# Kernel tuning notes

Hardware: AMD Instinct MI355X
Metric: run time of the kernel (lower is better)

The kernel has to match this reference:

```python
import jax, jax.numpy as jnp
import numpy as np
from jax import lax

D_MODEL = 1024
D_INNER = 2048   # expand * d_model
D_STATE = 16
D_CONV = 4
DT_RANK = 64     # ceil(d_model / 16)
B_SZ, L_SEQ = 2, 2048


def setup_inputs() -> dict:
    key = jax.random.key(0)
    ks = jax.random.split(key, 12)
    s = lambda *sh: 1.0 / np.sqrt(sh[-1])
    inp = {
        "x": jax.random.normal(ks[0], (B_SZ, L_SEQ, D_MODEL), jnp.float32),
        "in_proj_w": jax.random.normal(ks[1], (2 * D_INNER, D_MODEL), jnp.float32) * s(D_MODEL),
        "conv_w": jax.random.normal(ks[2], (D_INNER, 1, D_CONV), jnp.float32) * 0.3,
        "conv_b": jax.random.normal(ks[3], (D_INNER,), jnp.float32) * 0.05,
        "x_proj_w": jax.random.normal(ks[4], (DT_RANK + 2 * D_STATE, D_INNER), jnp.float32) * s(D_INNER),
        "dt_proj_w": jax.random.normal(ks[5], (D_INNER, DT_RANK), jnp.float32) * s(DT_RANK),
        "dt_proj_b": jnp.log(jnp.exp(jax.random.uniform(ks[6], (D_INNER,), jnp.float32, 1e-3, 1e-1)) - 1.0),
        "A_log": jnp.log(jnp.broadcast_to(jnp.arange(1, D_STATE + 1, dtype=jnp.float32), (D_INNER, D_STATE))),
        "D": jnp.ones((D_INNER,), jnp.float32),
        "out_proj_w": jax.random.normal(ks[7], (D_MODEL, D_INNER), jnp.float32) * s(D_INNER),
        "ln_w": jnp.ones((D_MODEL,), jnp.float32),
        "ln_b": jnp.zeros((D_MODEL,), jnp.float32),
    }
    return inp


def _mamba(x, in_proj_w, conv_w, conv_b, x_proj_w, dt_proj_w, dt_proj_b, A_log, D, out_proj_w):
    # x: [B, L, d_model]
    xz = x @ in_proj_w.T                             # [B, L, 2*d_inner]
    u, z = jnp.split(xz, 2, axis=-1)                 # [B, L, d_inner] each
    # depthwise causal conv1d along L
    u_c = jnp.swapaxes(u, 1, 2)                      # [B, d_inner, L]
    u_c = lax.conv_general_dilated(
        u_c, conv_w, window_strides=(1,), padding=[(D_CONV - 1, 0)],
        feature_group_count=D_INNER, dimension_numbers=("NCH", "OIH", "NCH"))
    u_c = u_c + conv_b[None, :, None]
    u_c = jax.nn.silu(jnp.swapaxes(u_c, 1, 2))       # [B, L, d_inner]
    # input-dependent dt, B, C
    x_dbl = u_c @ x_proj_w.T                         # [B, L, dt_rank + 2*d_state]
    dt_lr = x_dbl[..., :DT_RANK]
    Bm = x_dbl[..., DT_RANK:DT_RANK + D_STATE]       # [B, L, d_state]
    Cm = x_dbl[..., DT_RANK + D_STATE:]              # [B, L, d_state]
    dt = jax.nn.softplus(dt_lr @ dt_proj_w.T + dt_proj_b)  # [B, L, d_inner]
    A = -jnp.exp(A_log)                              # [d_inner, d_state]

    def step(h, inputs):
        dt_t, b_t, c_t, u_t = inputs                 # [B,d_inner],[B,N],[B,N],[B,d_inner]
        dA = jnp.exp(dt_t[:, :, None] * A)           # [B, d_inner, N]
        h = h * dA + (dt_t * u_t)[:, :, None] * b_t[:, None, :]
        y_t = jnp.einsum("bdn,bn->bd", h, c_t)
        return h, y_t

    h0 = jnp.zeros((x.shape[0], D_INNER, D_STATE), x.dtype)
    xs = (jnp.swapaxes(dt, 0, 1), jnp.swapaxes(Bm, 0, 1),
          jnp.swapaxes(Cm, 0, 1), jnp.swapaxes(u_c, 0, 1))
    _, ys = lax.scan(step, h0, xs)                   # ys: [L, B, d_inner]
    y = jnp.swapaxes(ys, 0, 1) + u_c * D             # skip connection D*u
    y = y * jax.nn.silu(z)                           # gate
    return y @ out_proj_w.T                          # [B, L, d_model]


def _layernorm(x, w, b, eps=1e-5):
    mu = jnp.mean(x, axis=-1, keepdims=True)
    var = jnp.mean(jnp.square(x - mu), axis=-1, keepdims=True)
    return (x - mu) * lax.rsqrt(var + eps) * w + b


def reference(x, in_proj_w, conv_w, conv_b, x_proj_w, dt_proj_w, dt_proj_b,
              A_log, D, out_proj_w, ln_w, ln_b):
    y = _mamba(x, in_proj_w, conv_w, conv_b, x_proj_w, dt_proj_w, dt_proj_b,
               A_log, D, out_proj_w)
    return _layernorm(y + x, ln_w, ln_b)  # dropout_level=0 -> identity
```

## Files before the change

kernel.cpp:

```cpp
#include <hip/hip_runtime.h>
#include <hip/hip_bf16.h>
#include <math.h>

#define DEV static __device__ __forceinline__

typedef __hip_bfloat16 bf16;
typedef __attribute__((ext_vector_type(8))) short bf16x8;
typedef __attribute__((ext_vector_type(4))) short bf16x4;
typedef __attribute__((ext_vector_type(4))) float f32x4;

static constexpr int D_MODEL = 1024;
static constexpr int D_INNER = 2048;
static constexpr int D_STATE = 16;
static constexpr int DT_RANK = 64;
static constexpr int B_SZ   = 2;
static constexpr int L_SEQ  = 2048;
static constexpr int T_TOK  = B_SZ * L_SEQ;
static constexpr int LC     = 64;
static constexpr int NC     = L_SEQ / LC;
static constexpr int NXP    = DT_RANK + 2 * D_STATE;
static constexpr int KSPLIT = 8;

static constexpr int P_CONVW = 0;
static constexpr int P_CONVB = 8192;
static constexpr int P_DTB   = 10240;
static constexpr int P_ALOG  = 12288;
static constexpr int P_DW    = 45056;
static constexpr int P_LNW   = 47104;
static constexpr int P_LNB   = 48128;
static constexpr int P_TOT   = 49152;

DEV float bf2f(bf16 x) { return __bfloat162float(x); }
DEV bf16  f2bf(float x) { return __float2bfloat16(x); }
DEV float sigmoidf_(float x) { return 1.0f / (1.0f + __expf(-x)); }
DEV float s2f(short s) { bf16 b; __builtin_memcpy(&b, &s, 2); return bf2f(b); }
DEV short f2s(float x) { bf16 b = f2bf(x); short s; __builtin_memcpy(&s, &b, 2); return s; }

DEV bool probe_f32(const unsigned short* probe) { return probe[1] == 0; }

DEV void async_copy16(const void* g, void* l) {
  __builtin_amdgcn_global_load_lds(
      (const __attribute__((address_space(1))) void*)g,
      (__attribute__((address_space(3))) void*)l, 16, 0, 0);
}

template <int N>
DEV void vm_wait() {
  if constexpr (N == 6) asm volatile("s_waitcnt vmcnt(6)" ::: "memory");
  else                  asm volatile("s_waitcnt vmcnt(0)" ::: "memory");
}

__global__ void cvt_all(const void* s0, const void* s1, const void* s2,
                        const void* s3, const void* s4,
                        const void* s5, const void* s6, const void* s7,
                        const void* s8, const void* s9, const void* s10,
                        const void* s11,
                        bf16* d0, bf16* d1, bf16* d2, bf16* d3, bf16* d4,
                        float* params,
                        const unsigned short* __restrict__ probe)
{
  long i = (long)(blockIdx.x * 256 + threadIdx.x) * 8;
  const void* src; long off;
  bf16* dstb = nullptr; float* dstf = nullptr;
  if      (i <  4194304) { src = s0;  dstb = d0; off = i; }
  else if (i <  8388608) { src = s1;  dstb = d1; off = i - 4194304; }
  else if (i <  8585216) { src = s2;  dstb = d2; off = i - 8388608; }
  else if (i <  8716288) { src = s3;  dstb = d3; off = i - 8585216; }
  else if (i < 10813440) { src = s4;  dstb = d4; off = i - 8716288; }
  else if (i < 10821632) { src = s5;  dstf = params + P_CONVW; off = i - 10813440; }
  else if (i < 10823680) { src = s6;  dstf = params + P_CONVB; off = i - 10821632; }
  else if (i < 10825728) { src = s7;  dstf = params + P_DTB;   off = i - 10823680; }
  else if (i < 10858496) { src = s8;  dstf = params + P_ALOG;  off = i - 10825728; }
  else if (i < 10860544) { src = s9;  dstf = params + P_DW;    off = i - 10858496; }
  else if (i < 10861568) { src = s10; dstf = params + P_LNW;   off = i - 10860544; }
  else if (i < 10862592) { src = s11; dstf = params + P_LNB;   off = i - 10861568; }
  else return;
  bool isf32 = probe_f32(probe);
  float v[8];
  if (isf32) {
    float4 a = *(const float4*)((const float*)src + off);
    float4 b = *(const float4*)((const float*)src + off + 4);
    v[0]=a.x; v[1]=a.y; v[2]=a.z; v[3]=a.w;
    v[4]=b.x; v[5]=b.y; v[6]=b.z; v[7]=b.w;
  } else {
    bf16x8 t = *(const bf16x8*)((const bf16*)src + off);
    #pragma unroll
    for (int k = 0; k < 8; ++k) { short sk = t[k]; v[k] = s2f(sk); }
  }
  if (dstb) {
    bf16x8 o;
    #pragma unroll
    for (int k = 0; k < 8; ++k) o[k] = f2s(v[k]);
    *(bf16x8*)(dstb + off) = o;
  } else {
    f32x4 a = {v[0], v[1], v[2], v[3]};
    f32x4 b = {v[4], v[5], v[6], v[7]};
    *(f32x4*)(dstf + off)     = a;
    *(f32x4*)(dstf + off + 4) = b;
  }
}

static constexpr int SLOT = 48 * 1024;
static constexpr int BOFF = 32 * 1024;

DEV void stage_A(const bf16* __restrict__ A, int ld, int bm, int k0,
                 char* slot, int tid) {
  #pragma unroll
  for (int j = 0; j < 4; ++j) {
    int p   = j * 8192 + tid * 16;
    int row = p >> 7;
    int ck  = ((p >> 4) & 7) ^ (row & 7);
    async_copy16(A + (size_t)(bm + row) * ld + k0 + ck * 8,
                 slot + j * 8192 + (tid >> 6) * 1024);
  }
}

DEV void stage_B(const bf16* __restrict__ B, int ld, int bn, int k0,
                 char* slot, int tid) {
  #pragma unroll
  for (int j = 0; j < 2; ++j) {
    int p   = j * 8192 + tid * 16;
    int row = p >> 7;
    int ck  = ((p >> 4) & 7) ^ (row & 7);
    async_copy16(B + (size_t)(bn + row) * ld + k0 + ck * 8,
                 slot + BOFF + j * 8192 + (tid >> 6) * 1024);
  }
}

template <int MODE>
DEV void gemm_pipe(const bf16* __restrict__ A, const bf16* __restrict__ B,
                   int M, int K, int ld,
                   void* __restrict__ o0, void* __restrict__ o1,
                   const float* __restrict__ cw, const float* __restrict__ cb,
                   bf16* __restrict__ ufirst, bf16* __restrict__ ulast)
{
  __shared__ __align__(16) char ring[3 * SLOT];
  if (MODE == 3) {
    A += (size_t)blockIdx.z * K;
    B += (size_t)blockIdx.z * K;
  }
  const int tid  = threadIdx.x;
  const int wave = tid >> 6;
  const int lane = tid & 63;
  const int bm = blockIdx.x * 256;
  const int bn = blockIdx.y * 128;
  const int wm = (wave >> 1) * 64;
  const int wn = (wave & 1) * 64;
  const int fr = lane & 15;
  const int fq = lane >> 4;
  const int NT = K / 64;

  f32x4 acc[4][4];
  #pragma unroll
  for (int i = 0; i < 4; ++i)
    #pragma unroll
    for (int j = 0; j < 4; ++j)
      #pragma unroll
      for (int r = 0; r < 4; ++r) acc[i][j][r] = 0.0f;

  stage_A(A, ld, bm, 0,  ring,        tid);
  stage_B(B, ld, bn, 0,  ring,        tid);
  stage_A(A, ld, bm, 64, ring + SLOT, tid);
  stage_B(B, ld, bn, 64, ring + SLOT, tid);

  int scur = 0;
  #pragma unroll 1
  for (int tk = 0; tk < NT; ++tk) {
    if (tk < NT - 1) vm_wait<6>();
    else             vm_wait<0>();
    __builtin_amdgcn_sched_barrier(0);
    __builtin_amdgcn_s_barrier();
    __builtin_amdgcn_sched_barrier(0);

    const char* sa = ring + scur * SLOT;
    int snxt = scur + 2; if (snxt >= 3) snxt -= 3;
    char* sn = ring + snxt * SLOT;

    bf16x8 af[4][2], bg[2][2];
    #pragma unroll
    for (int mi = 0; mi < 4; ++mi)
      #pragma unroll
      for (int kk = 0; kk < 2; ++kk) {
        int row = wm + mi * 16 + fr;
        af[mi][kk] = *(const bf16x8*)(sa + row * 128 + (((kk * 4 + fq) ^ (fr & 7)) * 16));
      }
    #pragma unroll
    for (int ni = 0; ni < 2; ++ni)
      #pragma unroll
      for (int kk = 0; kk < 2; ++kk) {
        int row = wn + ni * 16 + fr;
        bg[ni][kk] = *(const bf16x8*)(sa + BOFF + row * 128 + (((kk * 4 + fq) ^ (fr & 7)) * 16));
      }
    __builtin_amdgcn_sched_barrier(0);
    if (tk + 2 < NT) stage_A(A, ld, bm, (tk + 2) * 64, sn, tid);
    __builtin_amdgcn_sched_barrier(0);
    asm volatile("s_waitcnt lgkmcnt(0)" ::: "memory");
    __builtin_amdgcn_sched_barrier(0);
    __builtin_amdgcn_s_setprio(1);
    #pragma unroll
    for (int kk = 0; kk < 2; ++kk)
      #pragma unroll
      for (int mi = 0; mi < 4; ++mi)
        #pragma unroll
        for (int ni = 0; ni < 2; ++ni)
          acc[mi][ni] = __builtin_amdgcn_mfma_f32_16x16x32_bf16(af[mi][kk], bg[ni][kk], acc[mi][ni], 0, 0, 0);
    __builtin_amdgcn_s_setprio(0);
    __builtin_amdgcn_sched_barrier(0);

    bf16x8 bh[2][2];
    #pragma unroll
    for (int ni = 0; ni < 2; ++ni)
      #pragma unroll
      for (int kk = 0; kk < 2; ++kk) {
        int row = wn + (ni + 2) * 16 + fr;
        bh[ni][kk] = *(const bf16x8*)(sa + BOFF + row * 128 + (((kk * 4 + fq) ^ (fr & 7)) * 16));
      }
    __builtin_amdgcn_sched_barrier(0);
    if (tk + 2 < NT) stage_B(B, ld, bn, (tk + 2) * 64, sn, tid);
    __builtin_amdgcn_sched_barrier(0);
    asm volatile("s_waitcnt lgkmcnt(0)" ::: "memory");
    __builtin_amdgcn_sched_barrier(0);
    __builtin_amdgcn_s_setprio(1);
    #pragma unroll
    for (int kk = 0; kk < 2; ++kk)
      #pragma unroll
      for (int mi = 0; mi < 4; ++mi)
        #pragma unroll
        for (int ni = 0; ni < 2; ++ni)
          acc[mi][ni + 2] = __builtin_amdgcn_mfma_f32_16x16x32_bf16(af[mi][kk], bh[ni][kk], acc[mi][ni + 2], 0, 0, 0);
    __builtin_amdgcn_s_setprio(0);
    __builtin_amdgcn_sched_barrier(0);

    scur = (scur + 1 == 3) ? 0 : scur + 1;
  }

  const int er = (lane >> 4) * 4;
  const int ec = lane & 15;

  if (MODE == 3) {
    #pragma unroll
    for (int mi = 0; mi < 4; ++mi)
      #pragma unroll
      for (int ni = 0; ni < 4; ++ni)
        #pragma unroll
        for (int r = 0; r < 4; ++r) {
          int row = bm + wm + mi * 16 + er + r;
          int col = bn + wn + ni * 16 + ec;
          ((bf16*)o0)[((size_t)blockIdx.z * M + row) * D_MODEL + col] = f2bf(acc[mi][ni][r]);
        }
    return;
  }

  if (bn >= D_INNER) {
    #pragma unroll
    for (int mi = 0; mi < 4; ++mi)
      #pragma unroll
      for (int ni = 0; ni < 4; ++ni)
        #pragma unroll
        for (int r = 0; r < 4; ++r) {
          int row = bm + wm + mi * 16 + er + r;
          int col = bn + wn + ni * 16 + ec - D_INNER;
          float v = acc[mi][ni][r];
          ((bf16*)o1)[(size_t)row * D_INNER + col] = f2bf(v * sigmoidf_(v));
        }
    return;
  }

  __syncthreads();
  bf16*  uT  = (bf16*)ring;
  float* cws = (float*)(ring + 70656);
  float* cbs = (float*)(ring + 72704);

  #pragma unroll
  for (int mi = 0; mi < 4; ++mi)
    #pragma unroll
    for (int ni = 0; ni < 4; ++ni)
      #pragma unroll
      for (int r = 0; r < 4; ++r)
        uT[(size_t)(wm + mi * 16 + er + r) * 136 + wn + ni * 16 + ec] = f2bf(acc[mi][ni][r]);

  if (tid < 128) {
    *(f32x4*)(cws + tid * 4) = *(const f32x4*)(cw + (size_t)(bn + tid) * 4);
    cbs[tid] = cb[bn + tid];
  }
  __syncthreads();

  if (tid < 48) {
    int i  = tid >> 4;
    int c8 = (tid & 15) * 8;
    size_t hb = ((size_t)(bm >> 8) * 3 + i) * D_INNER + bn + c8;
    *(bf16x8*)(ufirst + hb) = *(const bf16x8*)(uT + (size_t)i * 136 + c8);
    *(bf16x8*)(ulast  + hb) = *(const bf16x8*)(uT + (size_t)(253 + i) * 136 + c8);
  }

  const int cg = tid & 15;
  float cwr[4][8], cbr[8];
  #pragma unroll
  for (int i = 0; i < 8; ++i) {
    f32x4 w4 = *(const f32x4*)(cws + (cg * 8 + i) * 4);
    cwr[0][i] = w4[0]; cwr[1][i] = w4[1]; cwr[2][i] = w4[2]; cwr[3][i] = w4[3];
    cbr[i] = cbs[cg * 8 + i];
  }
  const int lbase = bm & (L_SEQ - 1);
  #pragma unroll
  for (int j = 0; j < 8; ++j) {
    int row = (tid >> 4) + j * 32;
    if (row < 3 && lbase != 0) continue;
    float a8[8];
    #pragma unroll
    for (int i = 0; i < 8; ++i) a8[i] = cbr[i];
    #pragma unroll
    for (int w = 0; w < 4; ++w) {
      if (row - 3 + w >= 0) {
        bf16x8 u8 = *(const bf16x8*)(uT + (size_t)(row - 3 + w) * 136 + cg * 8);
        #pragma unroll
        for (int i = 0; i < 8; ++i) { short uu = u8[i]; a8[i] += s2f(uu) * cwr[w][i]; }
      }
    }
    bf16x8 o;
    #pragma unroll
    for (int i = 0; i < 8; ++i) o[i] = f2s(a8[i] * sigmoidf_(a8[i]));
    *(bf16x8*)((bf16*)o0 + (size_t)(bm + row) * D_INNER + bn + cg * 8) = o;
  }
}

__global__ void __launch_bounds__(256) k_convfix(
    const bf16* __restrict__ ufirst, const bf16* __restrict__ ulast,
    const float* __restrict__ cw, const float* __restrict__ cb,
    bf16* __restrict__ uc_bf)
{
  int idx = blockIdx.x * 256 + threadIdx.x;
  int e4 = idx * 4;
  int ti = e4 >> 11;
  int c4 = e4 & 2047;
  int tb = ti / 3, r = ti - tb * 3;
  int rb = (tb < 7) ? tb + 1 : tb + 2;
  int token = rb * 256 + r;
  float a[4];
  float4 wv[4];
  #pragma unroll
  for (int i = 0; i < 4; ++i) {
    a[i]  = cb[c4 + i];
    wv[i] = *(const float4*)(cw + (size_t)(c4 + i) * 4);
  }
  #pragma unroll
  for (int w = 0; w < 4; ++w) {
    int g = r - 3 + w;
    const bf16* srcrow = (g < 0)
        ? (ulast  + ((size_t)(rb - 1) * 3 + (g + 3)) * D_INNER)
        : (ufirst + ((size_t)rb * 3 + g) * D_INNER);
    bf16x4 u = *(const bf16x4*)(srcrow + c4);
    #pragma unroll
    for (int i = 0; i < 4; ++i) { short su = u[i]; a[i] += s2f(su) * ((const float*)&wv[i])[w]; }
  }
  bf16x4 o;
  #pragma unroll
  for (int i = 0; i < 4; ++i) o[i] = f2s(a[i] * sigmoidf_(a[i]));
  *(bf16x4*)(uc_bf + (size_t)token * D_INNER + c4) = o;
}

__global__ void __launch_bounds__(256) k_xproj(const bf16* __restrict__ A,
                                               const bf16* __restrict__ B,
                                               float* __restrict__ o0)
{
  __shared__ __align__(16) bf16 As[128 * 32];
  __shared__ __align__(16) bf16 Bs[128 * 32];
  const int M = T_TOK, N = NXP, K = D_INNER / KSPLIT, ld = D_INNER;
  A += (size_t)blockIdx.z * K;
  B += (size_t)blockIdx.z * K;
  const int tid  = threadIdx.x;
  const int wave = tid >> 6;
  const int lane = tid & 63;
  const int bm = blockIdx.x * 128;
  const int bn = 0;
  const int wm = (wave >> 1) * 64;
  const int wn = (wave & 1) * 64;

  f32x4 acc[4][4];
  #pragma unroll
  for (int i = 0; i < 4; ++i)
    #pragma unroll
    for (int j = 0; j < 4; ++j)
      #pragma unroll
      for (int r = 0; r < 4; ++r) acc[i][j][r] = 0.0f;

  const int ar0 = tid >> 2;
  const int ar1 = ar0 + 64;
  const int ac  = (tid & 3) * 8;
  const int fr = lane & 15;
  const int fk = (lane >> 4) * 8;

  for (int k0 = 0; k0 < K; k0 += 32) {
    bf16x8 a0 = *(const bf16x8*)(A + (size_t)(bm + ar0) * ld + k0 + ac);
    bf16x8 a1 = *(const bf16x8*)(A + (size_t)(bm + ar1) * ld + k0 + ac);
    int r0 = bn + ar0; if (r0 > N - 1) r0 = N - 1;
    int r1 = bn + ar1; if (r1 > N - 1) r1 = N - 1;
    bf16x8 b0 = *(const bf16x8*)(B + (size_t)r0 * ld + k0 + ac);
    bf16x8 b1 = *(const bf16x8*)(B + (size_t)r1 * ld + k0 + ac);
    __syncthreads();
    *(bf16x8*)(As + ar0 * 32 + ac) = a0;
    *(bf16x8*)(As + ar1 * 32 + ac) = a1;
    *(bf16x8*)(Bs + ar0 * 32 + ac) = b0;
    *(bf16x8*)(Bs + ar1 * 32 + ac) = b1;
    __syncthreads();

    bf16x8 af[4], bg[4];
    #pragma unroll
    for (int mi = 0; mi < 4; ++mi)
      af[mi] = *(const bf16x8*)(As + (wm + mi * 16 + fr) * 32 + fk);
    #pragma unroll
    for (int ni = 0; ni < 4; ++ni)
      bg[ni] = *(const bf16x8*)(Bs + (wn + ni * 16 + fr) * 32 + fk);
    #pragma unroll
    for (int mi = 0; mi < 4; ++mi)
      #pragma unroll
      for (int ni = 0; ni < 4; ++ni)
        acc[mi][ni] = __builtin_amdgcn_mfma_f32_16x16x32_bf16(af[mi], bg[ni], acc[mi][ni], 0, 0, 0);
  }

  const int er = (lane >> 4) * 4;
  const int ec = lane & 15;
  #pragma unroll
  for (int mi = 0; mi < 4; ++mi)
    #pragma unroll
    for (int ni = 0; ni < 4; ++ni)
      #pragma unroll
      for (int r = 0; r < 4; ++r) {
        int row = bm + wm + mi * 16 + er + r;
        int col = bn + wn + ni * 16 + ec;
        if (col >= N) continue;
        o0[((size_t)blockIdx.z * M + row) * N + col] = acc[mi][ni][r];
      }
}

__global__ void __launch_bounds__(512) k_inproj(const bf16* A, const bf16* B,
    void* o0, void* o1, const float* cw, const float* cb,
    bf16* ufirst, bf16* ulast) {
  gemm_pipe<0>(A, B, T_TOK, D_MODEL, D_MODEL, o0, o1, cw, cb, ufirst, ulast);
}
__global__ void __launch_bounds__(512) k_outproj(const bf16* A, const bf16* B,
    void* o0) {
  gemm_pipe<3>(A, B, T_TOK, D_INNER / 2, D_INNER, o0, nullptr, nullptr, nullptr,
               nullptr, nullptr);
}

__global__ __launch_bounds__(256) void k_dtfuse(
    const float* __restrict__ partials,
    const bf16*  __restrict__ dtw,
    const float* __restrict__ dtbias,
    float* __restrict__ Bbuf, float* __restrict__ Cbuf,
    bf16* __restrict__ dtb)
{
  __shared__ __align__(16) bf16 Al[128 * 72];
  __shared__ __align__(16) bf16 Bl[128 * 72];
  const int tid = threadIdx.x;
  unsigned lin = blockIdx.x + gridDim.x * blockIdx.y;
  unsigned nid = (lin & 7) * 64 + (lin >> 3);
  const int cblk = nid & 15;
  const int tblk = nid >> 4;
  const int r0 = tblk * 128;
  const int c0 = cblk * 128;

  #pragma unroll
  for (int it = 0; it < 8; ++it) {
    int idx = it * 256 + tid;
    int row = idx >> 4;
    int g   = idx & 15;
    f32x4 s = {0.0f, 0.0f, 0.0f, 0.0f};
    #pragma unroll
    for (int kz = 0; kz < KSPLIT; ++kz)
      s += *(const f32x4*)(partials + ((size_t)kz * T_TOK + r0 + row) * NXP + g * 4);
    bf16x4 o;
    #pragma unroll
    for (int k = 0; k < 4; ++k) o[k] = f2s(s[k]);
    *(bf16x4*)(Al + row * 72 + g * 4) = o;
  }
  if (cblk == 0) {
    #pragma unroll
    for (int it = 0; it < 4; ++it) {
      int idx = it * 256 + tid;
      int row = idx >> 3;
      int g   = 16 + (idx & 7);
      f32x4 s = {0.0f, 0.0f, 0.0f, 0.0f};
      #pragma unroll
      for (int kz = 0; kz < KSPLIT; ++kz)
        s += *(const f32x4*)(partials + ((size_t)kz * T_TOK + r0 + row) * NXP + g * 4);
      if (g < 20) *(f32x4*)(Bbuf + (size_t)(r0 + row) * D_STATE + (g - 16) * 4) = s;
      else        *(f32x4*)(Cbuf + (size_t)(r0 + row) * D_STATE + (g - 20) * 4) = s;
    }
  }
  #pragma unroll
  for (int it = 0; it < 4; ++it) {
    int idx = it * 256 + tid;
    int row = idx >> 3;
    int cv  = (idx & 7) * 8;
    *(bf16x8*)(Bl + row * 72 + cv) = *(const bf16x8*)(dtw + (size_t)(c0 + row) * 64 + cv);
  }
  __syncthreads();

  const int wave = tid >> 6;
  const int lane = tid & 63;
  const int wm = (wave >> 1) * 64;
  const int wn = (wave & 1) * 64;
  const int fr = lane & 15;
  const int fk = (lane >> 4) * 8;
  const int er = (lane >> 4) * 4;
  const int ec = lane & 15;

  f32x4 acc[4][4];
  #pragma unroll
  for (int i = 0; i < 4; ++i)
    #pragma unroll
    for (int j = 0; j < 4; ++j)
      #pragma unroll
      for (int r = 0; r < 4; ++r) acc[i][j][r] = 0.0f;

  #pragma unroll
  for (int k0 = 0; k0 < 64; k0 += 32) {
    bf16x8 af[4], bg[4];
    #pragma unroll
    for (int mi = 0; mi < 4; ++mi)
      af[mi] = *(const bf16x8*)(Al + (wm + mi * 16 + fr) * 72 + k0 + fk);
    #pragma unroll
    for (int ni = 0; ni < 4; ++ni)
      bg[ni] = *(const bf16x8*)(Bl + (wn + ni * 16 + fr) * 72 + k0 + fk);
    #pragma unroll
    for (int mi = 0; mi < 4; ++mi)
      #pragma unroll
      for (int ni = 0; ni < 4; ++ni)
        acc[mi][ni] = __builtin_amdgcn_mfma_f32_16x16x32_bf16(af[mi], bg[ni], acc[mi][ni], 0, 0, 0);
  }

  #pragma unroll
  for (int mi = 0; mi < 4; ++mi)
    #pragma unroll
    for (int ni = 0; ni < 4; ++ni)
      #pragma unroll
      for (int r = 0; r < 4; ++r) {
        int orow = r0 + wm + mi * 16 + er + r;
        int ocol = c0 + wn + ni * 16 + ec;
        float v = acc[mi][ni][r] + dtbias[ocol];
        float sp = (v > 15.0f) ? v : __logf(1.0f + __expf(v));
        dtb[(size_t)orow * D_INNER + ocol] = f2bf(sp);
      }
}

DEV void load_Ad(const float* A_log, int d, float* Ad, bool& fast) {
  fast = true;
  #pragma unroll
  for (int n = 0; n < 16; ++n) {
    Ad[n] = -__expf(A_log[d * 16 + n]);
    fast = fast && (fabsf(Ad[n] + (float)(n + 1)) < 1e-3f * (n + 1));
  }
}
DEV void compute_decay(bool fast, float dtv, const float* Ad, float* dec) {
  if (fast) {
    float e1 = __expf(-dtv);
    float en = e1;
    #pragma unroll
    for (int n = 0; n < 16; ++n) { dec[n] = en; en *= e1; }
  } else {
    #pragma unroll
    for (int n = 0; n < 16; ++n) dec[n] = __expf(Ad[n] * dtv);
  }
}

__global__ __launch_bounds__(256) void scan_pass1(
    const bf16* __restrict__ dt, const bf16* __restrict__ uc_bf,
    const float* __restrict__ Bbuf, const float* __restrict__ A_log,
    float* __restrict__ hend, float* __restrict__ sumdt)
{
  __shared__ float Bs4[LC * D_STATE];
  __shared__ bf16 dts[16 * 256];
  __shared__ bf16 uts[16 * 256];
  int bid = blockIdx.x;
  int tid = threadIdx.x;
  int dt8 = bid & 7;
  int c = (bid >> 3) & (NC - 1);
  int b = bid >> 8;
  int d0 = dt8 * 256;
  int d  = d0 + tid;
  int t0g = b * L_SEQ + c * LC;

  ((f32x4*)Bs4)[tid] = ((const f32x4*)(Bbuf + (size_t)t0g * D_STATE))[tid];

  float Ad[16], h[16];
  bool fast;
  load_Ad(A_log, d, Ad, fast);
  #pragma unroll
  for (int n = 0; n < 16; ++n) h[n] = 0.0f;
  float sdt = 0.0f;

  for (int sub = 0; sub < 4; ++sub) {
    __syncthreads();
    #pragma unroll
    for (int rep = 0; rep < 2; ++rep) {
      int idx = rep * 256 + tid;
      int row = idx >> 5;
      int col = (idx & 31) * 8;
      size_t src = (size_t)(t0g + sub * 16 + row) * D_INNER + d0 + col;
      *(bf16x8*)(dts + row * 256 + col) = *(const bf16x8*)(dt + src);
      *(bf16x8*)(uts + row * 256 + col) = *(const bf16x8*)(uc_bf + src);
    }
    __syncthreads();
    for (int t = 0; t < 16; ++t) {
      float dtv = bf2f(dts[t * 256 + tid]);
      float uv  = bf2f(uts[t * 256 + tid]);
      float su  = dtv * uv;
      sdt += dtv;
      float dec[16];
      compute_decay(fast, dtv, Ad, dec);
      const float* Bp = Bs4 + (sub * 16 + t) * 16;
      #pragma unroll
      for (int n = 0; n < 16; ++n)
        h[n] = h[n] * dec[n] + su * Bp[n];
    }
  }
  size_t base = ((size_t)(b * NC + c) * D_INNER + d) * 16;
  #pragma unroll
  for (int q = 0; q < 4; ++q)
    *(f32x4*)(hend + base + q * 4) = *(f32x4*)(h + q * 4);
  sumdt[(size_t)(b * NC + c) * D_INNER + d] = sdt;
}

__global__ __launch_bounds__(256) void scan_pass2(
    float* __restrict__ hend, const float* __restrict__ sumdt,
    const float* __restrict__ A_log)
{
  __shared__ float Ms[4][64];
  __shared__ float Es[4][64];
  int bid = blockIdx.x;
  int tid = threadIdx.x;
  int cg   = tid >> 6;
  int lane = tid & 63;
  int dloc = lane >> 4;
  int n    = lane & 15;
  int b     = bid >> 9;
  int d     = (bid & 511) * 4 + dloc;

  float a = -__expf(A_log[d * 16 + n]);

  float Ml[8], El[8];
  float M = 1.0f, E = 0.0f;
  #pragma unroll
  for (int j = 0; j < 8; ++j) {
    int c = cg * 8 + j;
    size_t sbase = (size_t)(b * NC + c) * D_INNER + d;
    float m = __expf(a * sumdt[sbase]);
    float e = hend[sbase * 16 + n];
    Ml[j] = M; El[j] = E;
    M = m * M;
    E = m * E + e;
  }
  Ms[cg][lane] = M;
  Es[cg][lane] = E;
  __syncthreads();
  float Ep = 0.0f;
  for (int g = 0; g < cg; ++g) {
    float Mg = Ms[g][lane], Eg = Es[g][lane];
    Ep = Mg * Ep + Eg;
  }
  #pragma unroll
  for (int j = 0; j < 8; ++j) {
    int c = cg * 8 + j;
    size_t sbase = (size_t)(b * NC + c) * D_INNER + d;
    hend[sbase * 16 + n] = Ml[j] * Ep + El[j];
  }
}

__global__ __launch_bounds__(256) void scan_pass3(
    const bf16* __restrict__ dt, const bf16* __restrict__ uc_bf,
    const float* __restrict__ Bbuf, const float* __restrict__ Cbuf,
    const bf16* __restrict__ z_silu, const float* __restrict__ hstart,
    const float* __restrict__ A_log, const float* __restrict__ Dw,
    bf16* __restrict__ y_bf)
{
  __shared__ float Bs4[LC * D_STATE];
  __shared__ float Cs4[LC * D_STATE];
  __shared__ bf16 dts[16 * 256];
  __shared__ bf16 uts[16 * 256];
  __shared__ bf16 zts[16 * 256];
  int bid = blockIdx.x;
  int tid = threadIdx.x;
  int dt8 = bid & 7;
  int c = (bid >> 3) & (NC - 1);
  int b = bid >> 8;
  int d0 = dt8 * 256;
  int d  = d0 + tid;
  int t0g = b * L_SEQ + c * LC;

  ((f32x4*)Bs4)[tid] = ((const f32x4*)(Bbuf + (size_t)t0g * D_STATE))[tid];
  ((f32x4*)Cs4)[tid] = ((const f32x4*)(Cbuf + (size_t)t0g * D_STATE))[tid];

  float Ad[16], h[16];
  bool fast;
  load_Ad(A_log, d, Ad, fast);
  size_t base = ((size_t)(b * NC + c) * D_INNER + d) * 16;
  #pragma unroll
  for (int q = 0; q < 4; ++q)
    *(f32x4*)(h + q * 4) = *(const f32x4*)(hstart + base + q * 4);
  float Dv = Dw[d];

  for (int sub = 0; sub < 4; ++sub) {
    __syncthreads();
    #pragma unroll
    for (int rep = 0; rep < 2; ++rep) {
      int idx = rep * 256 + tid;
      int row = idx >> 5;
      int col = (idx & 31) * 8;
      size_t src = (size_t)(t0g + sub * 16 + row) * D_INNER + d0 + col;
      *(bf16x8*)(dts + row * 256 + col) = *(const bf16x8*)(dt + src);
      *(bf16x8*)(uts + row * 256 + col) = *(const bf16x8*)(uc_bf + src);
      *(bf16x8*)(zts + row * 256 + col) = *(const bf16x8*)(z_silu + src);
    }
    __syncthreads();
    for (int t = 0; t < 16; ++t) {
      float dtv = bf2f(dts[t * 256 + tid]);
      float uv  = bf2f(uts[t * 256 + tid]);
      float zv  = bf2f(zts[t * 256 + tid]);
      float su  = dtv * uv;
      float dec[16];
      compute_decay(fast, dtv, Ad, dec);
      const float* Bp = Bs4 + (sub * 16 + t) * 16;
      const float* Cp = Cs4 + (sub * 16 + t) * 16;
      float y = 0.0f;
      #pragma unroll
      for (int n = 0; n < 16; ++n) {
        h[n] = h[n] * dec[n] + su * Bp[n];
        y += h[n] * Cp[n];
      }
      y = (y + uv * Dv) * zv;
      y_bf[(size_t)(t0g + sub * 16 + t) * D_INNER + d] = f2bf(y);
    }
  }
}

__global__ void ln_kernel(const bf16* __restrict__ parts,
                          const bf16* __restrict__ x_bf,
                          const float* __restrict__ w,
                          const float* __restrict__ bia,
                          void* __restrict__ out,
                          const unsigned short* __restrict__ probe)
{
  int t = blockIdx.x;
  int tid = threadIdx.x;
  const bf16* p0 = parts + (size_t)t * D_MODEL;
  const bf16* p1 = parts + ((size_t)T_TOK + t) * D_MODEL;
  const bf16* xr = x_bf + (size_t)t * D_MODEL;
  float v[4];
  float s = 0.0f, q = 0.0f;
  #pragma unroll
  for (int k = 0; k < 4; ++k) {
    int col = tid + k * 256;
    v[k] = bf2f(p0[col]) + bf2f(p1[col]) + bf2f(xr[col]);
    s += v[k]; q += v[k] * v[k];
  }
  #pragma unroll
  for (int off = 32; off >= 1; off >>= 1) {
    s += __shfl_down(s, off);
    q += __shfl_down(q, off);
  }
  __shared__ float red[8];
  __shared__ float mv[2];
  int wave = tid >> 6, lane = tid & 63;
  if (lane == 0) { red[wave] = s; red[4 + wave] = q; }
  __syncthreads();
  if (tid == 0) {
    float S = red[0] + red[1] + red[2] + red[3];
    float Q = red[4] + red[5] + red[6] + red[7];
    float mu = S * (1.0f / D_MODEL);
    float var = Q * (1.0f / D_MODEL) - mu * mu;
    mv[0] = mu; mv[1] = rsqrtf(var + 1e-5f);
  }
  __syncthreads();
  float mu = mv[0], rs = mv[1];
  bool isf32 = probe_f32(probe);
  #pragma unroll
  for (int k = 0; k < 4; ++k) {
    int col = tid + k * 256;
    float r = (v[k] - mu) * rs * w[col] + bia[col];
    if (isf32) ((float*)out)[(size_t)t * D_MODEL + col] = r;
    else       ((bf16*) out)[(size_t)t * D_MODEL + col] = f2bf(r);
  }
}

extern "C" void kernel_launch(void* const* d_in, const int* in_sizes, int n_in,
                              void* d_out, int out_size, void* d_ws, size_t ws_size,
                              hipStream_t stream)
{
  const void* x        = d_in[0];
  const void* in_w     = d_in[1];
  const void* conv_w   = d_in[2];
  const void* conv_b   = d_in[3];
  const void* xproj_w  = d_in[4];
  const void* dtproj_w = d_in[5];
  const void* dtproj_b = d_in[6];
  const void* A_log    = d_in[7];
  const void* Dw       = d_in[8];
  const void* out_w    = d_in[9];
  const void* ln_w     = d_in[10];
  const void* ln_b     = d_in[11];
  const unsigned short* probe = (const unsigned short*)A_log;

  char* p = (char*)d_ws;
  auto alloc = [&](size_t bytes) { char* r = p; p += (bytes + 255) & ~255ull; return r; };
  bf16*  x_bf   = (bf16*) alloc((size_t)T_TOK * D_MODEL * 2);
  bf16*  inw_bf = (bf16*) alloc((size_t)2 * D_INNER * D_MODEL * 2);
  bf16*  xpw_bf = (bf16*) alloc((size_t)NXP * D_INNER * 2);
  bf16*  dtw_bf = (bf16*) alloc((size_t)D_INNER * DT_RANK * 2);
  bf16*  outw_bf= (bf16*) alloc((size_t)D_MODEL * D_INNER * 2);
  float* params = (float*)alloc((size_t)P_TOT * 4);
  bf16*  scratch= (bf16*) alloc((size_t)T_TOK * D_INNER * 2);
  bf16*  z_silu = (bf16*) alloc((size_t)T_TOK * D_INNER * 2);
  bf16*  uc_bf  = (bf16*) alloc((size_t)T_TOK * D_INNER * 2);
  float* Bbuf   = (float*)alloc((size_t)T_TOK * D_STATE * 4);
  float* Cbuf   = (float*)alloc((size_t)T_TOK * D_STATE * 4);
  bf16*  dtb    = (bf16*) alloc((size_t)T_TOK * D_INNER * 2);
  float* hend   = (float*)alloc((size_t)B_SZ * NC * D_INNER * 16 * 4);
  float* sumdt  = (float*)alloc((size_t)B_SZ * NC * D_INNER * 4);
  bf16*  ufirst = (bf16*) alloc((size_t)16 * 3 * D_INNER * 2);
  bf16*  ulast  = (bf16*) alloc((size_t)16 * 3 * D_INNER * 2);
  float* xparts = (float*)scratch;
  bf16*  y_bf   = scratch;
  bf16*  oparts = z_silu;

  dim3 blk(256);
  dim3 blk512(512);
  cvt_all<<<5304, blk, 0, stream>>>(x, in_w, xproj_w, dtproj_w, out_w,
                                    conv_w, conv_b, dtproj_b, A_log, Dw, ln_w, ln_b,
                                    x_bf, inw_bf, xpw_bf, dtw_bf, outw_bf, params, probe);

  k_inproj<<<dim3(T_TOK / 256, (2 * D_INNER) / 128), blk512, 0, stream>>>(
      x_bf, inw_bf, uc_bf, z_silu, params + P_CONVW, params + P_CONVB, ufirst, ulast);
  k_convfix<<<84, blk, 0, stream>>>(ufirst, ulast, params + P_CONVW, params + P_CONVB, uc_bf);
  k_xproj<<<dim3(T_TOK / 128, 1, KSPLIT), blk, 0, stream>>>(uc_bf, xpw_bf, xparts);
  k_dtfuse<<<dim3(16, 32), blk, 0, stream>>>(xparts, dtw_bf, params + P_DTB, Bbuf, Cbuf, dtb);
  scan_pass1<<<B_SZ * NC * (D_INNER / 256), blk, 0, stream>>>(dtb, uc_bf, Bbuf, params + P_ALOG, hend, sumdt);
  scan_pass2<<<(B_SZ * D_INNER) / 2, blk, 0, stream>>>(hend, sumdt, params + P_ALOG);
  scan_pass3<<<B_SZ * NC * (D_INNER / 256), blk, 0, stream>>>(
      dtb, uc_bf, Bbuf, Cbuf, z_silu, hend, params + P_ALOG, params + P_DW, y_bf);
  k_outproj<<<dim3(T_TOK / 256, D_MODEL / 128, 2), blk512, 0, stream>>>(y_bf, outw_bf, oparts);
  ln_kernel<<<T_TOK, blk, 0, stream>>>(oparts, x_bf, params + P_LNW, params + P_LNB, d_out, probe);
}
```

Before: 268.0 us.

## Fuse conv boundary fix into xproj and dtfuse; vectorize layernorm

Drops the separate k_convfix launch. The xproj GEMM now recomputes the causal-conv and SiLU values for the 3 boundary rows of each 256-token block on the fly. The dtfuse kernel writes those corrected rows back into uc_bf for the later scan passes. The layernorm kernel is also switched to vectorized 4-wide loads and stores. This saves one kernel launch and its serialization, at the cost of divergent extra work in some xproj and dtfuse blocks.

```diff
diff --git a/kernel.cpp b/kernel.cpp
--- a/kernel.cpp
+++ b/kernel.cpp
@@ -324,50 +324,20 @@
   }
 }
 
-__global__ void __launch_bounds__(256) k_convfix(
-    const bf16* __restrict__ ufirst, const bf16* __restrict__ ulast,
-    const float* __restrict__ cw, const float* __restrict__ cb,
-    bf16* __restrict__ uc_bf)
-{
-  int idx = blockIdx.x * 256 + threadIdx.x;
-  int e4 = idx * 4;
-  int ti = e4 >> 11;
-  int c4 = e4 & 2047;
-  int tb = ti / 3, r = ti - tb * 3;
-  int rb = (tb < 7) ? tb + 1 : tb + 2;
-  int token = rb * 256 + r;
-  float a[4];
-  float4 wv[4];
-  #pragma unroll
-  for (int i = 0; i < 4; ++i) {
-    a[i]  = cb[c4 + i];
-    wv[i] = *(const float4*)(cw + (size_t)(c4 + i) * 4);
-  }
-  #pragma unroll
-  for (int w = 0; w < 4; ++w) {
-    int g = r - 3 + w;
-    const bf16* srcrow = (g < 0)
-        ? (ulast  + ((size_t)(rb - 1) * 3 + (g + 3)) * D_INNER)
-        : (ufirst + ((size_t)rb * 3 + g) * D_INNER);
-    bf16x4 u = *(const bf16x4*)(srcrow + c4);
-    #pragma unroll
-    for (int i = 0; i < 4; ++i) { short su = u[i]; a[i] += s2f(su) * ((const float*)&wv[i])[w]; }
-  }
-  bf16x4 o;
-  #pragma unroll
-  for (int i = 0; i < 4; ++i) o[i] = f2s(a[i] * sigmoidf_(a[i]));
-  *(bf16x4*)(uc_bf + (size_t)token * D_INNER + c4) = o;
-}
-
 __global__ void __launch_bounds__(256) k_xproj(const bf16* __restrict__ A,
                                                const bf16* __restrict__ B,
-                                               float* __restrict__ o0)
+                                               float* __restrict__ o0,
+                                               const bf16* __restrict__ ufirst,
+                                               const bf16* __restrict__ ulast,
+                                               const float* __restrict__ cw,
+                                               const float* __restrict__ cb)
 {
   __shared__ __align__(16) bf16 As[128 * 32];
   __shared__ __align__(16) bf16 Bs[128 * 32];
   const int M = T_TOK, N = NXP, K = D_INNER / KSPLIT, ld = D_INNER;
-  A += (size_t)blockIdx.z * K;
-  B += (size_t)blockIdx.z * K;
+  const int zb = blockIdx.z * K;
+  A += (size_t)zb;
+  B += (size_t)zb;
   const int tid  = threadIdx.x;
   const int wave = tid >> 6;
   const int lane = tid & 63;
@@ -390,8 +360,33 @@
   const int fr = lane & 15;
   const int fk = (lane >> 4) * 8;
 
+  const bool fixr = ((bm & 255) == 0) && ((bm & (L_SEQ - 1)) != 0) && (ar0 < 3);
+  const int rb = bm >> 8;
+
   for (int k0 = 0; k0 < K; k0 += 32) {
-    bf16x8 a0 = *(const bf16x8*)(A + (size_t)(bm + ar0) * ld + k0 + ac);
+    bf16x8 a0;
+    if (fixr) {
+      float a8[8];
+      #pragma unroll
+      for (int i = 0; i < 8; ++i) a8[i] = cb[zb + k0 + ac + i];
+      #pragma unroll
+      for (int w = 0; w < 4; ++w) {
+        int g = ar0 - 3 + w;
+        const bf16* srow = (g < 0)
+            ? (ulast  + ((size_t)(rb - 1) * 3 + (g + 3)) * D_INNER)
+            : (ufirst + ((size_t)rb * 3 + g) * D_INNER);
+        bf16x8 u8 = *(const bf16x8*)(srow + zb + k0 + ac);
+        #pragma unroll
+        for (int i = 0; i < 8; ++i) {
+          short uu = u8[i];
+          a8[i] += s2f(uu) * cw[(size_t)(zb + k0 + ac + i) * 4 + w];
+        }
+      }
+      #pragma unroll
+      for (int i = 0; i < 8; ++i) a0[i] = f2s(a8[i] * sigmoidf_(a8[i]));
+    } else {
+      a0 = *(const bf16x8*)(A + (size_t)(bm + ar0) * ld + k0 + ac);
+    }
     bf16x8 a1 = *(const bf16x8*)(A + (size_t)(bm + ar1) * ld + k0 + ac);
     int r0 = bn + ar0; if (r0 > N - 1) r0 = N - 1;
     int r1 = bn + ar1; if (r1 > N - 1) r1 = N - 1;
@@ -449,7 +444,10 @@
     const bf16*  __restrict__ dtw,
     const float* __restrict__ dtbias,
     float* __restrict__ Bbuf, float* __restrict__ Cbuf,
-    bf16* __restrict__ dtb)
+    bf16* __restrict__ dtb,
+    const bf16* __restrict__ ufirst, const bf16* __restrict__ ulast,
+    const float* __restrict__ cw, const float* __restrict__ cb,
+    bf16* __restrict__ uc_bf)
 {
   __shared__ __align__(16) bf16 Al[128 * 72];
   __shared__ __align__(16) bf16 Bl[128 * 72];
@@ -460,6 +458,38 @@
   const int tblk = nid >> 4;
   const int r0 = tblk * 128;
   const int c0 = cblk * 128;
+
+  if (cblk == 1 && (tblk & 1) == 0) {
+    int rb = tblk >> 1;
+    if (rb >= 1 && rb < 16 && rb != 8) {
+      #pragma unroll
+      for (int it = 0; it < 6; ++it) {
+        int idx = it * 256 + tid;
+        int r  = idx / 512;
+        int c4 = (idx - r * 512) * 4;
+        float a[4]; float4 wv[4];
+        #pragma unroll
+        for (int i = 0; i < 4; ++i) {
+          a[i]  = cb[c4 + i];
+          wv[i] = *(const float4*)(cw + (size_t)(c4 + i) * 4);
+        }
+        #pragma unroll
+        for (int w = 0; w < 4; ++w) {
+          int g = r - 3 + w;
+          const bf16* srow = (g < 0)
+              ? (ulast  + ((size_t)(rb - 1) * 3 + (g + 3)) * D_INNER)
+              : (ufirst + ((size_t)rb * 3 + g) * D_INNER);
+          bf16x4 u = *(const bf16x4*)(srow + c4);
+          #pragma unroll
+          for (int i = 0; i < 4; ++i) { short su = u[i]; a[i] += s2f(su) * ((const float*)&wv[i])[w]; }
+        }
+        bf16x4 o;
+        #pragma unroll
+        for (int i = 0; i < 4; ++i) o[i] = f2s(a[i] * sigmoidf_(a[i]));
+        *(bf16x4*)(uc_bf + (size_t)(rb * 256 + r) * D_INNER + c4) = o;
+      }
+    }
+  }
 
   #pragma unroll
   for (int it = 0; it < 8; ++it) {
@@ -744,15 +774,19 @@
 {
   int t = blockIdx.x;
   int tid = threadIdx.x;
+  int c0 = tid * 4;
   const bf16* p0 = parts + (size_t)t * D_MODEL;
   const bf16* p1 = parts + ((size_t)T_TOK + t) * D_MODEL;
   const bf16* xr = x_bf + (size_t)t * D_MODEL;
+  bf16x4 va = *(const bf16x4*)(p0 + c0);
+  bf16x4 vb = *(const bf16x4*)(p1 + c0);
+  bf16x4 vx = *(const bf16x4*)(xr + c0);
   float v[4];
   float s = 0.0f, q = 0.0f;
   #pragma unroll
   for (int k = 0; k < 4; ++k) {
-    int col = tid + k * 256;
-    v[k] = bf2f(p0[col]) + bf2f(p1[col]) + bf2f(xr[col]);
+    short aa = va[k], bb = vb[k], xx = vx[k];
+    v[k] = s2f(aa) + s2f(bb) + s2f(xx);
     s += v[k]; q += v[k] * v[k];
   }
   #pragma unroll
@@ -775,12 +809,19 @@
   __syncthreads();
   float mu = mv[0], rs = mv[1];
   bool isf32 = probe_f32(probe);
-  #pragma unroll
-  for (int k = 0; k < 4; ++k) {
-    int col = tid + k * 256;
-    float r = (v[k] - mu) * rs * w[col] + bia[col];
-    if (isf32) ((float*)out)[(size_t)t * D_MODEL + col] = r;
-    else       ((bf16*) out)[(size_t)t * D_MODEL + col] = f2bf(r);
+  f32x4 wv = *(const f32x4*)(w + c0);
+  f32x4 bv = *(const f32x4*)(bia + c0);
+  float r[4];
+  #pragma unroll
+  for (int k = 0; k < 4; ++k) r[k] = (v[k] - mu) * rs * wv[k] + bv[k];
+  if (isf32) {
+    f32x4 o = {r[0], r[1], r[2], r[3]};
+    *(f32x4*)((float*)out + (size_t)t * D_MODEL + c0) = o;
+  } else {
+    bf16x4 o;
+    #pragma unroll
+    for (int k = 0; k < 4; ++k) o[k] = f2s(r[k]);
+    *(bf16x4*)((bf16*)out + (size_t)t * D_MODEL + c0) = o;
   }
 }
 
@@ -832,9 +873,11 @@
 
   k_inproj<<<dim3(T_TOK / 256, (2 * D_INNER) / 128), blk512, 0, stream>>>(
       x_bf, inw_bf, uc_bf, z_silu, params + P_CONVW, params + P_CONVB, ufirst, ulast);
-  k_convfix<<<84, blk, 0, stream>>>(ufirst, ulast, params + P_CONVW, params + P_CONVB, uc_bf);
-  k_xproj<<<dim3(T_TOK / 128, 1, KSPLIT), blk, 0, stream>>>(uc_bf, xpw_bf, xparts);
-  k_dtfuse<<<dim3(16, 32), blk, 0, stream>>>(xparts, dtw_bf, params + P_DTB, Bbuf, Cbuf, dtb);
+  k_xproj<<<dim3(T_TOK / 128, 1, KSPLIT), blk, 0, stream>>>(
+      uc_bf, xpw_bf, xparts, ufirst, ulast, params + P_CONVW, params + P_CONVB);
+  k_dtfuse<<<dim3(16, 32), blk, 0, stream>>>(
+      xparts, dtw_bf, params + P_DTB, Bbuf, Cbuf, dtb,
+      ufirst, ulast, params + P_CONVW, params + P_CONVB, uc_bf);
   scan_pass1<<<B_SZ * NC * (D_INNER / 256), blk, 0, stream>>>(dtb, uc_bf, Bbuf, params + P_ALOG, hend, sumdt);
   scan_pass2<<<(B_SZ * D_INNER) / 2, blk, 0, stream>>>(hend, sumdt, params + P_ALOG);
   scan_pass3<<<B_SZ * NC * (D_INNER / 256), blk, 0, stream>>>(
```

New measurement: 270.1 us. No clear change (+0.8%).

## Fold inter-chunk state propagation into scan pass3 and drop pass2 kernel

Applied to the files above, without the earlier changes.

Removes the separate scan_pass2 kernel that computed the carry-in state for each chunk. Instead, each scan_pass3 block recomputes its starting state by walking all preceding chunk end-states and decays serially. This saves one kernel launch and one round-trip of the hend buffer. In exchange, later chunks do redundant O(c) work, up to 31 extra chunk combines with exp per thread, which creates load imbalance across blocks.

```diff
diff --git a/kernel.cpp b/kernel.cpp
--- a/kernel.cpp
+++ b/kernel.cpp
@@ -623,55 +623,11 @@
   sumdt[(size_t)(b * NC + c) * D_INNER + d] = sdt;
 }
 
-__global__ __launch_bounds__(256) void scan_pass2(
-    float* __restrict__ hend, const float* __restrict__ sumdt,
-    const float* __restrict__ A_log)
-{
-  __shared__ float Ms[4][64];
-  __shared__ float Es[4][64];
-  int bid = blockIdx.x;
-  int tid = threadIdx.x;
-  int cg   = tid >> 6;
-  int lane = tid & 63;
-  int dloc = lane >> 4;
-  int n    = lane & 15;
-  int b     = bid >> 9;
-  int d     = (bid & 511) * 4 + dloc;
-
-  float a = -__expf(A_log[d * 16 + n]);
-
-  float Ml[8], El[8];
-  float M = 1.0f, E = 0.0f;
-  #pragma unroll
-  for (int j = 0; j < 8; ++j) {
-    int c = cg * 8 + j;
-    size_t sbase = (size_t)(b * NC + c) * D_INNER + d;
-    float m = __expf(a * sumdt[sbase]);
-    float e = hend[sbase * 16 + n];
-    Ml[j] = M; El[j] = E;
-    M = m * M;
-    E = m * E + e;
-  }
-  Ms[cg][lane] = M;
-  Es[cg][lane] = E;
-  __syncthreads();
-  float Ep = 0.0f;
-  for (int g = 0; g < cg; ++g) {
-    float Mg = Ms[g][lane], Eg = Es[g][lane];
-    Ep = Mg * Ep + Eg;
-  }
-  #pragma unroll
-  for (int j = 0; j < 8; ++j) {
-    int c = cg * 8 + j;
-    size_t sbase = (size_t)(b * NC + c) * D_INNER + d;
-    hend[sbase * 16 + n] = Ml[j] * Ep + El[j];
-  }
-}
-
 __global__ __launch_bounds__(256) void scan_pass3(
     const bf16* __restrict__ dt, const bf16* __restrict__ uc_bf,
     const float* __restrict__ Bbuf, const float* __restrict__ Cbuf,
-    const bf16* __restrict__ z_silu, const float* __restrict__ hstart,
+    const bf16* __restrict__ z_silu, const float* __restrict__ hend,
+    const float* __restrict__ sumdt,
     const float* __restrict__ A_log, const float* __restrict__ Dw,
     bf16* __restrict__ y_bf)
 {
@@ -695,10 +651,29 @@
   float Ad[16], h[16];
   bool fast;
   load_Ad(A_log, d, Ad, fast);
-  size_t base = ((size_t)(b * NC + c) * D_INNER + d) * 16;
-  #pragma unroll
-  for (int q = 0; q < 4; ++q)
-    *(f32x4*)(h + q * 4) = *(const f32x4*)(hstart + base + q * 4);
+
+  #pragma unroll
+  for (int n = 0; n < 16; ++n) h[n] = 0.0f;
+  #pragma unroll 1
+  for (int cp = 0; cp < c; ++cp) {
+    size_t sb = (size_t)(b * NC + cp) * D_INNER + d;
+    float s = sumdt[sb];
+    float dec[16];
+    compute_decay(fast, s, Ad, dec);
+    const float* he = hend + sb * 16;
+    f32x4 e0 = *(const f32x4*)(he);
+    f32x4 e1 = *(const f32x4*)(he + 4);
+    f32x4 e2 = *(const f32x4*)(he + 8);
+    f32x4 e3 = *(const f32x4*)(he + 12);
+    #pragma unroll
+    for (int n = 0; n < 4; ++n) h[n]      = h[n]      * dec[n]      + e0[n];
+    #pragma unroll
+    for (int n = 0; n < 4; ++n) h[n + 4]  = h[n + 4]  * dec[n + 4]  + e1[n];
+    #pragma unroll
+    for (int n = 0; n < 4; ++n) h[n + 8]  = h[n + 8]  * dec[n + 8]  + e2[n];
+    #pragma unroll
+    for (int n = 0; n < 4; ++n) h[n + 12] = h[n + 12] * dec[n + 12] + e3[n];
+  }
   float Dv = Dw[d];
 
   for (int sub = 0; sub < 4; ++sub) {
@@ -836,9 +811,8 @@
   k_xproj<<<dim3(T_TOK / 128, 1, KSPLIT), blk, 0, stream>>>(uc_bf, xpw_bf, xparts);
   k_dtfuse<<<dim3(16, 32), blk, 0, stream>>>(xparts, dtw_bf, params + P_DTB, Bbuf, Cbuf, dtb);
   scan_pass1<<<B_SZ * NC * (D_INNER / 256), blk, 0, stream>>>(dtb, uc_bf, Bbuf, params + P_ALOG, hend, sumdt);
-  scan_pass2<<<(B_SZ * D_INNER) / 2, blk, 0, stream>>>(hend, sumdt, params + P_ALOG);
   scan_pass3<<<B_SZ * NC * (D_INNER / 256), blk, 0, stream>>>(
-      dtb, uc_bf, Bbuf, Cbuf, z_silu, hend, params + P_ALOG, params + P_DW, y_bf);
+      dtb, uc_bf, Bbuf, Cbuf, z_silu, hend, sumdt, params + P_ALOG, params + P_DW, y_bf);
   k_outproj<<<dim3(T_TOK / 256, D_MODEL / 128, 2), blk512, 0, stream>>>(y_bf, outw_bf, oparts);
   ln_kernel<<<T_TOK, blk, 0, stream>>>(oparts, x_bf, params + P_LNW, params + P_LNB, d_out, probe);
 }
```

Measured after the change: 285.8 us. 1.07x slower.
